# Kernel tuning notes

Measured on AMD Instinct MI355X. Metric: run time of the kernel, lower is better.

Reference implementation:

```python
import jax, jax.numpy as jnp
import numpy as np

N = 50000   # nodes
E = 800000  # edges (before self loops)
NEG_SLOPE = 0.2
EPS_BN = 1e-5
EPS_SM = 1e-16  # PyG softmax denominator epsilon


def gat_conv(x, src, dst, W, att_src, att_dst, bias, heads, ch):
    n = x.shape[0]
    xh = (x @ W).reshape(n, heads, ch)                       # [N,H,C]
    a_src = jnp.sum(xh * att_src, axis=-1)                   # [N,H]
    a_dst = jnp.sum(xh * att_dst, axis=-1)                   # [N,H]
    e = a_src[src] + a_dst[dst]                              # [E,H]
    e = jax.nn.leaky_relu(e, NEG_SLOPE)
    m = jax.ops.segment_max(e, dst, num_segments=n)          # segment softmax
    ex = jnp.exp(e - m[dst])
    denom = jax.ops.segment_sum(ex, dst, num_segments=n)
    alpha = ex / (denom[dst] + EPS_SM)                       # [E,H]
    msg = alpha[:, :, None] * xh[src]                        # [E,H,C]
    out = jax.ops.segment_sum(msg, dst, num_segments=n)      # [N,H,C]
    return out.reshape(n, heads * ch) + bias


def batch_norm(x, gamma, beta):
    mu = jnp.mean(x, axis=0)
    var = jnp.mean((x - mu) ** 2, axis=0)
    return (x - mu) * jax.lax.rsqrt(var + EPS_BN) * gamma + beta


def setup_inputs() -> dict:
    key = jax.random.key(0)
    ks = jax.random.split(key, 16)
    d = {}
    d['x'] = jax.random.normal(ks[0], (N, 128), jnp.float32)
    d['edge_index'] = jax.random.randint(ks[1], (2, E), 0, N, dtype=jnp.int64)
    d['W1'] = jax.random.normal(ks[2], (128, 256), jnp.float32) * 0.1
    d['as1'] = jax.random.normal(ks[3], (2, 128), jnp.float32) * 0.1
    d['ad1'] = jax.random.normal(ks[4], (2, 128), jnp.float32) * 0.1
    d['b1'] = jax.random.normal(ks[5], (256,), jnp.float32) * 0.1
    d['g1'] = jnp.ones((256,), jnp.float32)
    d['be1'] = jnp.zeros((256,), jnp.float32)
    d['W2'] = jax.random.normal(ks[6], (256, 128), jnp.float32) * 0.1
    d['as2'] = jax.random.normal(ks[7], (2, 64), jnp.float32) * 0.1
    d['ad2'] = jax.random.normal(ks[8], (2, 64), jnp.float32) * 0.1
    d['b2'] = jax.random.normal(ks[9], (128,), jnp.float32) * 0.1
    d['g2'] = jnp.ones((128,), jnp.float32)
    d['be2'] = jnp.zeros((128,), jnp.float32)
    d['W3'] = jax.random.normal(ks[10], (128, 128), jnp.float32) * 0.1
    d['as3'] = jax.random.normal(ks[11], (2, 64), jnp.float32) * 0.1
    d['ad3'] = jax.random.normal(ks[12], (2, 64), jnp.float32) * 0.1
    d['b3'] = jax.random.normal(ks[13], (128,), jnp.float32) * 0.1
    d['lw'] = jax.random.normal(ks[14], (128, 64), jnp.float32) * 0.1
    d['lb'] = jnp.zeros((64,), jnp.float32)
    return d


def reference(x, edge_index, W1, as1, ad1, b1, g1, be1,
              W2, as2, ad2, b2, g2, be2,
              W3, as3, ad3, b3, lw, lb):
    # add self loops (PyG GATConv default add_self_loops=True)
    loops = jnp.arange(N, dtype=edge_index.dtype)
    src = jnp.concatenate([edge_index[0], loops])
    dst = jnp.concatenate([edge_index[1], loops])

    h = jax.nn.relu(gat_conv(x, src, dst, W1, as1, ad1, b1, 2, 128))   # [N,256]
    h = batch_norm(h, g1, be1)
    h = jax.nn.relu(gat_conv(h, src, dst, W2, as2, ad2, b2, 2, 64))    # [N,128]
    h = batch_norm(h, g2, be2)
    h = jax.nn.relu(gat_conv(h, src, dst, W3, as3, ad3, b3, 2, 64))    # [N,128]
    return h @ lw + lb                                                 # [N,64]
```

## Files before the change

kernel.cpp:

```cpp
#include <hip/hip_runtime.h>
#include <hip/hip_bf16.h>

#define NEG_SLOPE 0.2f
#define EPS_BN 1e-5f
#define EPS_SM 1e-16f

typedef __bf16 bf16x8 __attribute__((ext_vector_type(8)));
typedef __bf16 bf16x4 __attribute__((ext_vector_type(4)));
typedef __bf16 bf16x2 __attribute__((ext_vector_type(2)));
typedef float floatx4 __attribute__((ext_vector_type(4)));

__device__ __forceinline__ float leaky(float x) { return x > 0.f ? x : NEG_SLOPE * x; }

__global__ void k_detect(const int* __restrict__ ei, int* __restrict__ cnt, int e) {
    int i = threadIdx.x + blockIdx.x * blockDim.x;
    if (i < 1024 && 2 * i + 1 < 2 * e) {
        if (ei[2 * i + 1] != 0) atomicAdd(cnt, 1);
    }
}

__global__ void k_hist(const int* __restrict__ ei, const int* __restrict__ cnt,
                       int* __restrict__ deg, int e) {
    int g = threadIdx.x + blockIdx.x * blockDim.x;
    if (g >= e) return;
    bool is64 = (*cnt) < 512;
    int d = is64 ? ei[2 * (e + g)] : ei[e + g];
    atomicAdd(&deg[d], 1);
}

__global__ __launch_bounds__(1024) void k_scan1(const int* __restrict__ deg,
                                                int* __restrict__ excl,
                                                int* __restrict__ bsum, int n) {
    __shared__ int sm[1024];
    int tid = threadIdx.x;
    int g = blockIdx.x * 1024 + tid;
    int v = (g < n) ? deg[g] : 0;
    sm[tid] = v;
    __syncthreads();
    for (int off = 1; off < 1024; off <<= 1) {
        int t = (tid >= off) ? sm[tid - off] : 0;
        __syncthreads();
        sm[tid] += t;
        __syncthreads();
    }
    if (g < n) excl[g] = sm[tid] - v;
    if (tid == 1023) bsum[blockIdx.x] = sm[1023];
}

__global__ void k_scan2(int* bsum, int nb) {
    if (threadIdx.x == 0 && blockIdx.x == 0) {
        int acc = 0;
        for (int i = 0; i < nb; ++i) { int v = bsum[i]; bsum[i] = acc; acc += v; }
    }
}

__global__ void k_scan3(const int* __restrict__ excl, const int* __restrict__ bsum,
                        int* __restrict__ rowptr, int n, int e) {
    int g = threadIdx.x + blockIdx.x * blockDim.x;
    if (g < n) rowptr[g] = excl[g] + bsum[g >> 10];
    if (g == 0) rowptr[n] = e;
}

__global__ void k_scatter(const int* __restrict__ ei, const int* __restrict__ cnt,
                          const int* __restrict__ rowptr, int* __restrict__ fill,
                          int* __restrict__ col, int e) {
    int g = threadIdx.x + blockIdx.x * blockDim.x;
    if (g >= e) return;
    bool is64 = (*cnt) < 512;
    int s = is64 ? ei[2 * g] : ei[g];
    int d = is64 ? ei[2 * (e + g)] : ei[e + g];
    int pos = rowptr[d] + atomicAdd(&fill[d], 1);
    col[pos] = s;
}

__global__ void k_wconv(const float* __restrict__ W, __bf16* __restrict__ Wb,
                        int kshift, int M, int total) {
    int idx = threadIdx.x + blockIdx.x * blockDim.x;
    if (idx >= total) return;
    int mm = idx >> kshift;
    int kk = idx & ((1 << kshift) - 1);
    Wb[idx] = (__bf16)W[(size_t)kk * M + mm];
}

__global__ void k_bn_prep(const float* __restrict__ sums, const float* __restrict__ sqs,
                          const float* __restrict__ g, const float* __restrict__ b,
                          float* __restrict__ scale, float* __restrict__ shift,
                          int n, int f) {
    int c = threadIdx.x;
    if (c >= f) return;
    float mean = sums[c] / n;
    float var = sqs[c] / n - mean * mean;
    float sc = g[c] * rsqrtf(var + EPS_BN);
    scale[c] = sc;
    shift[c] = b[c] - mean * sc;
}

template <int K, int LC, bool BF16IN>
__global__ __launch_bounds__(256) void k_gemm(const void* __restrict__ Ain,
                                              const __bf16* __restrict__ Bt,
                                              __bf16* __restrict__ Cb, int n, int M,
                                              const float* __restrict__ scale,
                                              const float* __restrict__ shift,
                                              const float* __restrict__ att_s,
                                              const float* __restrict__ att_d,
                                              float* __restrict__ asrc,
                                              float* __restrict__ adst) {
    __shared__ __align__(16) __bf16 As[128][72];
    __shared__ __align__(16) __bf16 Bs[128][72];
    const int row0 = blockIdx.y * 128, col0 = blockIdx.x * 128;
    const int lane = threadIdx.x & 63, w = threadIdx.x >> 6;
    const int m = lane & 15, quad = lane >> 4;
    floatx4 acc[2][8];
#pragma unroll
    for (int i = 0; i < 2; ++i)
#pragma unroll
        for (int j = 0; j < 8; ++j) acc[i][j] = (floatx4)0.f;

    const int sr = threadIdx.x >> 1;
    const int sk = (threadIdx.x & 1) * 32;

    for (int kc = 0; kc < K; kc += 64) {
        {
            int grow = row0 + sr;
            if (grow < n) {
                if (BF16IN) {
                    const __bf16* p = (const __bf16*)Ain + (size_t)grow * K + kc + sk;
#pragma unroll
                    for (int q = 0; q < 4; ++q) {
                        bf16x8 vv = *reinterpret_cast<const bf16x8*>(p + q * 8);
                        if (scale) {
                            const float* scp = scale + kc + sk + q * 8;
                            const float* shp = shift + kc + sk + q * 8;
                            bf16x8 r;
#pragma unroll
                            for (int e2 = 0; e2 < 8; ++e2)
                                r[e2] = (__bf16)((float)vv[e2] * scp[e2] + shp[e2]);
                            vv = r;
                        }
                        *reinterpret_cast<bf16x8*>(&As[sr][sk + q * 8]) = vv;
                    }
                } else {
                    const float* p = (const float*)Ain + (size_t)grow * K + kc + sk;
#pragma unroll
                    for (int q = 0; q < 8; ++q) {
                        float4 v = *reinterpret_cast<const float4*>(p + q * 4);
                        if (scale) {
                            int c = kc + sk + q * 4;
                            float4 sc = *reinterpret_cast<const float4*>(scale + c);
                            float4 sh = *reinterpret_cast<const float4*>(shift + c);
                            v.x = v.x * sc.x + sh.x; v.y = v.y * sc.y + sh.y;
                            v.z = v.z * sc.z + sh.z; v.w = v.w * sc.w + sh.w;
                        }
                        bf16x4 cv = {(__bf16)v.x, (__bf16)v.y, (__bf16)v.z, (__bf16)v.w};
                        *reinterpret_cast<bf16x4*>(&As[sr][sk + q * 4]) = cv;
                    }
                }
            } else {
#pragma unroll
                for (int q = 0; q < 4; ++q)
                    *reinterpret_cast<bf16x8*>(&As[sr][sk + q * 8]) = (bf16x8)(__bf16)0.f;
            }
        }
        {
            const __bf16* p = Bt + (size_t)(col0 + sr) * K + kc + sk;
#pragma unroll
            for (int q = 0; q < 4; ++q)
                *reinterpret_cast<bf16x8*>(&Bs[sr][sk + q * 8]) =
                    *reinterpret_cast<const bf16x8*>(p + q * 8);
        }
        __syncthreads();
#pragma unroll
        for (int ks = 0; ks < 64; ks += 32) {
            bf16x8 a0 = *reinterpret_cast<const bf16x8*>(&As[w * 32 + m][ks + quad * 8]);
            bf16x8 a1 = *reinterpret_cast<const bf16x8*>(&As[w * 32 + 16 + m][ks + quad * 8]);
#pragma unroll
            for (int nt = 0; nt < 8; ++nt) {
                bf16x8 b = *reinterpret_cast<const bf16x8*>(&Bs[nt * 16 + m][ks + quad * 8]);
                acc[0][nt] = __builtin_amdgcn_mfma_f32_16x16x32_bf16(a0, b, acc[0][nt], 0, 0, 0);
                acc[1][nt] = __builtin_amdgcn_mfma_f32_16x16x32_bf16(a1, b, acc[1][nt], 0, 0, 0);
            }
        }
        __syncthreads();
    }
#pragma unroll
    for (int mt = 0; mt < 2; ++mt)
#pragma unroll
        for (int nt = 0; nt < 8; ++nt)
#pragma unroll
            for (int r = 0; r < 4; ++r) {
                int row = row0 + w * 32 + mt * 16 + quad * 4 + r;
                if (row < n) Cb[(size_t)row * M + col0 + nt * 16 + m] = (__bf16)acc[mt][nt][r];
            }
    {
        float asv[8], adv[8];
#pragma unroll
        for (int nt = 0; nt < 8; ++nt) {
            int c = col0 + nt * 16 + m;
            asv[nt] = att_s[c];
            adv[nt] = att_d[c];
        }
#pragma unroll
        for (int mt = 0; mt < 2; ++mt)
#pragma unroll
            for (int r = 0; r < 4; ++r) {
                int row = row0 + w * 32 + mt * 16 + quad * 4 + r;
                if (LC == 7) {
                    float pa = 0.f, pb = 0.f;
#pragma unroll
                    for (int nt = 0; nt < 8; ++nt) {
                        float v = acc[mt][nt][r];
                        pa += v * asv[nt];
                        pb += v * adv[nt];
                    }
#pragma unroll
                    for (int off = 1; off <= 8; off <<= 1) {
                        pa += __shfl_xor(pa, off);
                        pb += __shfl_xor(pb, off);
                    }
                    if (m == 0 && row < n) {
                        int h = (col0 >> 7) & 1;
                        atomicAdd(asrc + 2 * row + h, pa);
                        atomicAdd(adst + 2 * row + h, pb);
                    }
                } else {
                    float p00 = 0.f, p01 = 0.f, p10 = 0.f, p11 = 0.f;
#pragma unroll
                    for (int nt = 0; nt < 8; ++nt) {
                        float v = acc[mt][nt][r];
                        if (nt < 4) { p00 += v * asv[nt]; p10 += v * adv[nt]; }
                        else        { p01 += v * asv[nt]; p11 += v * adv[nt]; }
                    }
#pragma unroll
                    for (int off = 1; off <= 8; off <<= 1) {
                        p00 += __shfl_xor(p00, off);
                        p01 += __shfl_xor(p01, off);
                        p10 += __shfl_xor(p10, off);
                        p11 += __shfl_xor(p11, off);
                    }
                    if (m == 0 && row < n) {
                        atomicAdd(asrc + 2 * row + 0, p00);
                        atomicAdd(asrc + 2 * row + 1, p01);
                        atomicAdd(adst + 2 * row + 0, p10);
                        atomicAdd(adst + 2 * row + 1, p11);
                    }
                }
            }
    }
}

__global__ __launch_bounds__(256) void k_lin(const float* __restrict__ A,
                                             const float* __restrict__ lw,
                                             const float* __restrict__ lb,
                                             float* __restrict__ out, int n) {
    __shared__ __align__(16) __bf16 Ahi[64][136];
    __shared__ __align__(16) __bf16 Alo[64][136];
    __shared__ __align__(16) __bf16 Bhi[64][136];
    const int row0 = blockIdx.x * 64;
    const int lane = threadIdx.x & 63, w = threadIdx.x >> 6;
    const int m = lane & 15, quad = lane >> 4;
    floatx4 acc[4];
#pragma unroll
    for (int i = 0; i < 4; ++i) acc[i] = (floatx4)0.f;

    {
        int sr = threadIdx.x >> 2, sk0 = (threadIdx.x & 3) * 32;
        int grow = row0 + sr;
#pragma unroll
        for (int q = 0; q < 8; ++q) {
            float4 v = make_float4(0.f, 0.f, 0.f, 0.f);
            if (grow < n) v = *reinterpret_cast<const float4*>(A + (size_t)grow * 128 + sk0 + q * 4);
            float vv[4] = {v.x, v.y, v.z, v.w};
#pragma unroll
            for (int i = 0; i < 4; ++i) {
                __bf16 h = (__bf16)vv[i];
                Ahi[sr][sk0 + q * 4 + i] = h;
                Alo[sr][sk0 + q * 4 + i] = (__bf16)(vv[i] - (float)h);
            }
        }
    }
    {
        int k0 = threadIdx.x >> 1, m0 = (threadIdx.x & 1) * 32;
#pragma unroll
        for (int q = 0; q < 8; ++q) {
            float4 v = *reinterpret_cast<const float4*>(lw + (size_t)k0 * 64 + m0 + q * 4);
            float vv[4] = {v.x, v.y, v.z, v.w};
#pragma unroll
            for (int i = 0; i < 4; ++i) Bhi[m0 + q * 4 + i][k0] = (__bf16)vv[i];
        }
    }
    __syncthreads();
#pragma unroll
    for (int ks = 0; ks < 128; ks += 32) {
        bf16x8 ah = *reinterpret_cast<const bf16x8*>(&Ahi[w * 16 + m][ks + quad * 8]);
        bf16x8 al = *reinterpret_cast<const bf16x8*>(&Alo[w * 16 + m][ks + quad * 8]);
#pragma unroll
        for (int nt = 0; nt < 4; ++nt) {
            bf16x8 bh = *reinterpret_cast<const bf16x8*>(&Bhi[nt * 16 + m][ks + quad * 8]);
            acc[nt] = __builtin_amdgcn_mfma_f32_16x16x32_bf16(ah, bh, acc[nt], 0, 0, 0);
            acc[nt] = __builtin_amdgcn_mfma_f32_16x16x32_bf16(al, bh, acc[nt], 0, 0, 0);
        }
    }
#pragma unroll
    for (int nt = 0; nt < 4; ++nt)
#pragma unroll
        for (int r = 0; r < 4; ++r) {
            int row = row0 + w * 16 + quad * 4 + r;
            int c = nt * 16 + m;
            if (row < n) out[(size_t)row * 64 + c] = acc[nt][r] + lb[c];
        }
}

template <int C, bool OUTBF16>
__global__ __launch_bounds__(256) void k_agg(const __bf16* __restrict__ xh,
                                             const float* __restrict__ asrc,
                                             const float* __restrict__ adst,
                                             const int* __restrict__ rowptr,
                                             const int* __restrict__ col,
                                             const float* __restrict__ bias,
                                             void* __restrict__ outv, int n) {
    constexpr int F = 2 * C;
    constexpr int VEC = F / 64;
    __shared__ float4 slots[4][64];
    const int widx = threadIdx.x >> 6;
    const int node = blockIdx.x * 4 + widx;
    const int lane = threadIdx.x & 63;
    if (node >= n) return;
    const bool h1 = (lane * VEC) >= C;
    const int beg = rowptr[node];
    const int deg = rowptr[node + 1] - beg;
    const float2 adv = *reinterpret_cast<const float2*>(adst + 2 * node);
    const float2 asv = *reinterpret_cast<const float2*>(asrc + 2 * node);
    const float es0 = leaky(asv.x + adv.x), es1 = leaky(asv.y + adv.y);
    float acc[VEC] = {};
    float d0 = 0.f, d1 = 0.f;

    for (int base = 0; base < deg; base += 64) {
        const int cnt = min(64, deg - base);
        if (lane < cnt) {
            int s = col[beg + base + lane];
            float2 av = *reinterpret_cast<const float2*>(asrc + 2 * s);
            float w0 = __expf(leaky(av.x + adv.x));
            float w1 = __expf(leaky(av.y + adv.y));
            d0 += w0; d1 += w1;
            slots[widx][lane] = make_float4(__int_as_float(s), w0, w1, 0.f);
        }
        int j = 0;
        for (; j + 4 <= cnt; j += 4) {
            float4 s0 = slots[widx][j + 0];
            float4 s1 = slots[widx][j + 1];
            float4 s2 = slots[widx][j + 2];
            float4 s3 = slots[widx][j + 3];
            const __bf16* p0 = xh + (size_t)__float_as_int(s0.x) * F + lane * VEC;
            const __bf16* p1 = xh + (size_t)__float_as_int(s1.x) * F + lane * VEC;
            const __bf16* p2 = xh + (size_t)__float_as_int(s2.x) * F + lane * VEC;
            const __bf16* p3 = xh + (size_t)__float_as_int(s3.x) * F + lane * VEC;
            if constexpr (VEC == 4) {
                bf16x4 v0 = *reinterpret_cast<const bf16x4*>(p0);
                bf16x4 v1 = *reinterpret_cast<const bf16x4*>(p1);
                bf16x4 v2 = *reinterpret_cast<const bf16x4*>(p2);
                bf16x4 v3 = *reinterpret_cast<const bf16x4*>(p3);
                float w0 = h1 ? s0.z : s0.y, w1 = h1 ? s1.z : s1.y;
                float w2 = h1 ? s2.z : s2.y, w3 = h1 ? s3.z : s3.y;
#pragma unroll
                for (int q = 0; q < 4; ++q)
                    acc[q] += w0 * (float)v0[q] + w1 * (float)v1[q] +
                              w2 * (float)v2[q] + w3 * (float)v3[q];
            } else {
                bf16x2 v0 = *reinterpret_cast<const bf16x2*>(p0);
                bf16x2 v1 = *reinterpret_cast<const bf16x2*>(p1);
                bf16x2 v2 = *reinterpret_cast<const bf16x2*>(p2);
                bf16x2 v3 = *reinterpret_cast<const bf16x2*>(p3);
                float w0 = h1 ? s0.z : s0.y, w1 = h1 ? s1.z : s1.y;
                float w2 = h1 ? s2.z : s2.y, w3 = h1 ? s3.z : s3.y;
#pragma unroll
                for (int q = 0; q < 2; ++q)
                    acc[q] += w0 * (float)v0[q] + w1 * (float)v1[q] +
                              w2 * (float)v2[q] + w3 * (float)v3[q];
            }
        }
        for (; j < cnt; ++j) {
            float4 s0 = slots[widx][j];
            const __bf16* p0 = xh + (size_t)__float_as_int(s0.x) * F + lane * VEC;
            float w0 = h1 ? s0.z : s0.y;
            if constexpr (VEC == 4) {
                bf16x4 v0 = *reinterpret_cast<const bf16x4*>(p0);
#pragma unroll
                for (int q = 0; q < 4; ++q) acc[q] += w0 * (float)v0[q];
            } else {
                bf16x2 v0 = *reinterpret_cast<const bf16x2*>(p0);
#pragma unroll
                for (int q = 0; q < 2; ++q) acc[q] += w0 * (float)v0[q];
            }
        }
    }
#pragma unroll
    for (int off = 1; off <= 32; off <<= 1) {
        d0 += __shfl_xor(d0, off);
        d1 += __shfl_xor(d1, off);
    }
    float exs0 = __expf(es0), exs1 = __expf(es1);
    d0 += exs0; d1 += exs1;
    {
        float ws = h1 ? exs1 : exs0;
        const __bf16* p = xh + (size_t)node * F + lane * VEC;
        if constexpr (VEC == 4) {
            bf16x4 v = *reinterpret_cast<const bf16x4*>(p);
#pragma unroll
            for (int q = 0; q < 4; ++q) acc[q] += ws * (float)v[q];
        } else {
            bf16x2 v = *reinterpret_cast<const bf16x2*>(p);
#pragma unroll
            for (int q = 0; q < 2; ++q) acc[q] += ws * (float)v[q];
        }
    }
    float inv = 1.0f / ((h1 ? d1 : d0) + EPS_SM);
    float o[VEC];
#pragma unroll
    for (int q = 0; q < VEC; ++q) o[q] = fmaxf(acc[q] * inv + bias[lane * VEC + q], 0.f);
    if constexpr (OUTBF16) {
        __bf16* po = (__bf16*)outv + (size_t)node * F + lane * VEC;
        if constexpr (VEC == 4) {
            bf16x4 st = {(__bf16)o[0], (__bf16)o[1], (__bf16)o[2], (__bf16)o[3]};
            *reinterpret_cast<bf16x4*>(po) = st;
        } else {
            bf16x2 st = {(__bf16)o[0], (__bf16)o[1]};
            *reinterpret_cast<bf16x2*>(po) = st;
        }
    } else {
        float* po = (float*)outv + (size_t)node * F + lane * VEC;
        if constexpr (VEC == 4) *reinterpret_cast<float4*>(po) = make_float4(o[0], o[1], o[2], o[3]);
        else                    *reinterpret_cast<float2*>(po) = make_float2(o[0], o[1]);
    }
}

template <typename T>
__global__ void k_bn_stats(const T* __restrict__ x, float* __restrict__ sums,
                           float* __restrict__ sqs, int n, int f) {
    int c = threadIdx.x;
    float s = 0.f, q = 0.f;
    for (int r = blockIdx.x; r < n; r += gridDim.x) {
        float v = (float)x[(size_t)r * f + c];
        s += v; q += v * v;
    }
    atomicAdd(&sums[c], s);
    atomicAdd(&sqs[c], q);
}

extern "C" void kernel_launch(void* const* d_in, const int* in_sizes, int n_in,
                              void* d_out, int out_size, void* d_ws, size_t ws_size,
                              hipStream_t stream) {
    const float* x   = (const float*)d_in[0];
    const int*   ei  = (const int*)d_in[1];
    const float* W1  = (const float*)d_in[2];
    const float* as1 = (const float*)d_in[3];
    const float* ad1 = (const float*)d_in[4];
    const float* b1  = (const float*)d_in[5];
    const float* g1  = (const float*)d_in[6];
    const float* be1 = (const float*)d_in[7];
    const float* W2  = (const float*)d_in[8];
    const float* as2 = (const float*)d_in[9];
    const float* ad2 = (const float*)d_in[10];
    const float* b2  = (const float*)d_in[11];
    const float* g2  = (const float*)d_in[12];
    const float* be2 = (const float*)d_in[13];
    const float* W3  = (const float*)d_in[14];
    const float* as3 = (const float*)d_in[15];
    const float* ad3 = (const float*)d_in[16];
    const float* b3  = (const float*)d_in[17];
    const float* lw  = (const float*)d_in[18];
    const float* lb  = (const float*)d_in[19];
    float* outp = (float*)d_out;

    const int n = in_sizes[0] / 128;
    const int e = in_sizes[1] / 2;

    char* w = (char*)d_ws;
    size_t off = 0;
    auto alloc = [&](size_t bytes) -> void* {
        void* p = w + off;
        off += (bytes + 255) & ~(size_t)255;
        return p;
    };
    __bf16* xhb = (__bf16*)alloc((size_t)n * 256 * 2);
    __bf16* h1b = (__bf16*)alloc((size_t)n * 256 * 2);
    __bf16* h2b = (__bf16*)alloc((size_t)n * 128 * 2);
    float*  h3f = (float*)alloc((size_t)n * 128 * 4);
    int* excl   = (int*)alloc((size_t)n * 4);
    int* rowptr = (int*)alloc((size_t)(n + 1) * 4);
    int* colb   = (int*)alloc((size_t)e * 4);
    int* bsum   = (int*)alloc(64 * 4);
    float* sc1  = (float*)alloc(256 * 4);
    float* sh1  = (float*)alloc(256 * 4);
    float* sc2  = (float*)alloc(128 * 4);
    float* sh2  = (float*)alloc(128 * 4);
    __bf16* Wb1 = (__bf16*)alloc(256 * 128 * 2);
    __bf16* Wb2 = (__bf16*)alloc(128 * 256 * 2);
    __bf16* Wb3 = (__bf16*)alloc(128 * 128 * 2);
    char* zb_begin = (char*)(w + off);
    int* deg    = (int*)alloc((size_t)n * 4);
    int* fill   = (int*)alloc((size_t)n * 4);
    float* bn1  = (float*)alloc(512 * 4);
    float* bn2  = (float*)alloc(512 * 4);
    int* dcnt   = (int*)alloc(256);
    float* as1p = (float*)alloc((size_t)n * 2 * 4);
    float* ad1p = (float*)alloc((size_t)n * 2 * 4);
    float* as2p = (float*)alloc((size_t)n * 2 * 4);
    float* ad2p = (float*)alloc((size_t)n * 2 * 4);
    float* as3p = (float*)alloc((size_t)n * 2 * 4);
    float* ad3p = (float*)alloc((size_t)n * 2 * 4);
    char* zb_end = (char*)(w + off);

    const int nb1 = (n + 1023) / 1024;

    hipMemsetAsync(zb_begin, 0, (size_t)(zb_end - zb_begin), stream);

    k_detect<<<4, 256, 0, stream>>>(ei, dcnt, e);
    k_hist<<<(e + 255) / 256, 256, 0, stream>>>(ei, dcnt, deg, e);
    k_scan1<<<nb1, 1024, 0, stream>>>(deg, excl, bsum, n);
    k_scan2<<<1, 1, 0, stream>>>(bsum, nb1);
    k_scan3<<<(n + 255) / 256, 256, 0, stream>>>(excl, bsum, rowptr, n, e);
    k_scatter<<<(e + 255) / 256, 256, 0, stream>>>(ei, dcnt, rowptr, fill, colb, e);

    k_wconv<<<(256 * 128 + 255) / 256, 256, 0, stream>>>(W1, Wb1, 7, 256, 256 * 128);
    k_wconv<<<(128 * 256 + 255) / 256, 256, 0, stream>>>(W2, Wb2, 8, 128, 128 * 256);
    k_wconv<<<(128 * 128 + 255) / 256, 256, 0, stream>>>(W3, Wb3, 7, 128, 128 * 128);

    const int nwb = (n + 3) / 4;
    const int nrow = (n + 127) / 128;

    k_gemm<128, 7, false><<<dim3(2, nrow), 256, 0, stream>>>(
        x, Wb1, xhb, n, 256, nullptr, nullptr, as1, ad1, as1p, ad1p);
    k_agg<128, true><<<nwb, 256, 0, stream>>>(xhb, as1p, ad1p, rowptr, colb, b1, h1b, n);
    k_bn_stats<__bf16><<<256, 256, 0, stream>>>(h1b, bn1, bn1 + 256, n, 256);
    k_bn_prep<<<1, 256, 0, stream>>>(bn1, bn1 + 256, g1, be1, sc1, sh1, n, 256);

    k_gemm<256, 6, true><<<dim3(1, nrow), 256, 0, stream>>>(
        h1b, Wb2, xhb, n, 128, sc1, sh1, as2, ad2, as2p, ad2p);
    k_agg<64, true><<<nwb, 256, 0, stream>>>(xhb, as2p, ad2p, rowptr, colb, b2, h2b, n);
    k_bn_stats<__bf16><<<256, 128, 0, stream>>>(h2b, bn2, bn2 + 256, n, 128);
    k_bn_prep<<<1, 256, 0, stream>>>(bn2, bn2 + 256, g2, be2, sc2, sh2, n, 128);

    k_gemm<128, 6, true><<<dim3(1, nrow), 256, 0, stream>>>(
        h2b, Wb3, xhb, n, 128, sc2, sh2, as3, ad3, as3p, ad3p);
    k_agg<64, false><<<nwb, 256, 0, stream>>>(xhb, as3p, ad3p, rowptr, colb, b3, h3f, n);

    k_lin<<<(n + 63) / 64, 256, 0, stream>>>(h3f, lw, lb, outp, n);
}
```

Measured before the change: 533.5 us.

## Vectorize GAT aggregation gathers and cut CSR/BN/weight-conversion launches

```diff
diff --git a/kernel.cpp b/kernel.cpp
--- a/kernel.cpp
+++ b/kernel.cpp
@@ -7,7 +7,6 @@
 
 typedef __bf16 bf16x8 __attribute__((ext_vector_type(8)));
 typedef __bf16 bf16x4 __attribute__((ext_vector_type(4)));
-typedef __bf16 bf16x2 __attribute__((ext_vector_type(2)));
 typedef float floatx4 __attribute__((ext_vector_type(4)));
 
 __device__ __forceinline__ float leaky(float x) { return x > 0.f ? x : NEG_SLOPE * x; }
@@ -20,12 +19,12 @@
 }
 
 __global__ void k_hist(const int* __restrict__ ei, const int* __restrict__ cnt,
-                       int* __restrict__ deg, int e) {
+                       int* __restrict__ deg, int* __restrict__ rnk, int e) {
     int g = threadIdx.x + blockIdx.x * blockDim.x;
     if (g >= e) return;
     bool is64 = (*cnt) < 512;
     int d = is64 ? ei[2 * (e + g)] : ei[e + g];
-    atomicAdd(&deg[d], 1);
+    rnk[g] = atomicAdd(&deg[d], 1);
 }
 
 __global__ __launch_bounds__(1024) void k_scan1(const int* __restrict__ deg,
@@ -47,69 +46,79 @@
     if (tid == 1023) bsum[blockIdx.x] = sm[1023];
 }
 
-__global__ void k_scan2(int* bsum, int nb) {
-    if (threadIdx.x == 0 && blockIdx.x == 0) {
-        int acc = 0;
-        for (int i = 0; i < nb; ++i) { int v = bsum[i]; bsum[i] = acc; acc += v; }
-    }
-}
-
 __global__ void k_scan3(const int* __restrict__ excl, const int* __restrict__ bsum,
                         int* __restrict__ rowptr, int n, int e) {
+    __shared__ int pref;
     int g = threadIdx.x + blockIdx.x * blockDim.x;
-    if (g < n) rowptr[g] = excl[g] + bsum[g >> 10];
+    if (threadIdx.x == 0) {
+        int chunk = (blockIdx.x * blockDim.x) >> 10;
+        int acc = 0;
+        for (int i = 0; i < chunk; ++i) acc += bsum[i];
+        pref = acc;
+    }
+    __syncthreads();
+    if (g < n) rowptr[g] = excl[g] + pref;
     if (g == 0) rowptr[n] = e;
 }
 
 __global__ void k_scatter(const int* __restrict__ ei, const int* __restrict__ cnt,
-                          const int* __restrict__ rowptr, int* __restrict__ fill,
+                          const int* __restrict__ rowptr, const int* __restrict__ rnk,
                           int* __restrict__ col, int e) {
     int g = threadIdx.x + blockIdx.x * blockDim.x;
     if (g >= e) return;
     bool is64 = (*cnt) < 512;
     int s = is64 ? ei[2 * g] : ei[g];
     int d = is64 ? ei[2 * (e + g)] : ei[e + g];
-    int pos = rowptr[d] + atomicAdd(&fill[d], 1);
-    col[pos] = s;
-}
-
-__global__ void k_wconv(const float* __restrict__ W, __bf16* __restrict__ Wb,
-                        int kshift, int M, int total) {
+    col[rowptr[d] + rnk[g]] = s;
+}
+
+__global__ void k_wconv(const float* __restrict__ W1, __bf16* __restrict__ Wb1,
+                        const float* __restrict__ W2, __bf16* __restrict__ Wb2,
+                        const float* __restrict__ W3, __bf16* __restrict__ Wb3) {
     int idx = threadIdx.x + blockIdx.x * blockDim.x;
-    if (idx >= total) return;
-    int mm = idx >> kshift;
-    int kk = idx & ((1 << kshift) - 1);
-    Wb[idx] = (__bf16)W[(size_t)kk * M + mm];
-}
-
-__global__ void k_bn_prep(const float* __restrict__ sums, const float* __restrict__ sqs,
-                          const float* __restrict__ g, const float* __restrict__ b,
-                          float* __restrict__ scale, float* __restrict__ shift,
-                          int n, int f) {
-    int c = threadIdx.x;
-    if (c >= f) return;
-    float mean = sums[c] / n;
-    float var = sqs[c] / n - mean * mean;
-    float sc = g[c] * rsqrtf(var + EPS_BN);
-    scale[c] = sc;
-    shift[c] = b[c] - mean * sc;
+    if (idx < 32768) {
+        int mm = idx >> 7, kk = idx & 127;
+        Wb1[idx] = (__bf16)W1[(size_t)kk * 256 + mm];
+    } else if (idx < 65536) {
+        int i2 = idx - 32768;
+        int mm = i2 >> 8, kk = i2 & 255;
+        Wb2[i2] = (__bf16)W2[(size_t)kk * 128 + mm];
+    } else if (idx < 81920) {
+        int i3 = idx - 65536;
+        int mm = i3 >> 7, kk = i3 & 127;
+        Wb3[i3] = (__bf16)W3[(size_t)kk * 128 + mm];
+    }
 }
 
 template <int K, int LC, bool BF16IN>
 __global__ __launch_bounds__(256) void k_gemm(const void* __restrict__ Ain,
                                               const __bf16* __restrict__ Bt,
                                               __bf16* __restrict__ Cb, int n, int M,
-                                              const float* __restrict__ scale,
-                                              const float* __restrict__ shift,
+                                              const float* __restrict__ bnsums,
+                                              const float* __restrict__ gam,
+                                              const float* __restrict__ bet,
                                               const float* __restrict__ att_s,
                                               const float* __restrict__ att_d,
                                               float* __restrict__ asrc,
                                               float* __restrict__ adst) {
     __shared__ __align__(16) __bf16 As[128][72];
     __shared__ __align__(16) __bf16 Bs[128][72];
+    __shared__ float sc_lds[K], sh_lds[K];
     const int row0 = blockIdx.y * 128, col0 = blockIdx.x * 128;
     const int lane = threadIdx.x & 63, w = threadIdx.x >> 6;
     const int m = lane & 15, quad = lane >> 4;
+
+    if (bnsums) {
+        for (int c = threadIdx.x; c < K; c += 256) {
+            float mean = bnsums[c] / n;
+            float var = bnsums[256 + c] / n - mean * mean;
+            float sc = gam[c] * rsqrtf(var + EPS_BN);
+            sc_lds[c] = sc;
+            sh_lds[c] = bet[c] - mean * sc;
+        }
+        __syncthreads();
+    }
+
     floatx4 acc[2][8];
 #pragma unroll
     for (int i = 0; i < 2; ++i)
@@ -128,13 +137,12 @@
 #pragma unroll
                     for (int q = 0; q < 4; ++q) {
                         bf16x8 vv = *reinterpret_cast<const bf16x8*>(p + q * 8);
-                        if (scale) {
-                            const float* scp = scale + kc + sk + q * 8;
-                            const float* shp = shift + kc + sk + q * 8;
+                        if (bnsums) {
+                            int c = kc + sk + q * 8;
                             bf16x8 r;
 #pragma unroll
                             for (int e2 = 0; e2 < 8; ++e2)
-                                r[e2] = (__bf16)((float)vv[e2] * scp[e2] + shp[e2]);
+                                r[e2] = (__bf16)((float)vv[e2] * sc_lds[c + e2] + sh_lds[c + e2]);
                             vv = r;
                         }
                         *reinterpret_cast<bf16x8*>(&As[sr][sk + q * 8]) = vv;
@@ -144,13 +152,6 @@
 #pragma unroll
                     for (int q = 0; q < 8; ++q) {
                         float4 v = *reinterpret_cast<const float4*>(p + q * 4);
-                        if (scale) {
-                            int c = kc + sk + q * 4;
-                            float4 sc = *reinterpret_cast<const float4*>(scale + c);
-                            float4 sh = *reinterpret_cast<const float4*>(shift + c);
-                            v.x = v.x * sc.x + sh.x; v.y = v.y * sc.y + sh.y;
-                            v.z = v.z * sc.z + sh.z; v.w = v.w * sc.w + sh.w;
-                        }
                         bf16x4 cv = {(__bf16)v.x, (__bf16)v.y, (__bf16)v.z, (__bf16)v.w};
                         *reinterpret_cast<bf16x4*>(&As[sr][sk + q * 4]) = cv;
                     }
@@ -261,7 +262,6 @@
     floatx4 acc[4];
 #pragma unroll
     for (int i = 0; i < 4; ++i) acc[i] = (floatx4)0.f;
-
     {
         int sr = threadIdx.x >> 2, sk0 = (threadIdx.x & 3) * 32;
         int grow = row0 + sr;
@@ -319,117 +319,86 @@
                                              const float* __restrict__ bias,
                                              void* __restrict__ outv, int n) {
     constexpr int F = 2 * C;
-    constexpr int VEC = F / 64;
-    __shared__ float4 slots[4][64];
+    constexpr int G = F / 8;
+    constexpr int NG = 64 / G;
+    constexpr int GSH = (G == 32) ? 5 : 4;
+    __shared__ float4 slots[4][72];
     const int widx = threadIdx.x >> 6;
     const int node = blockIdx.x * 4 + widx;
     const int lane = threadIdx.x & 63;
     if (node >= n) return;
-    const bool h1 = (lane * VEC) >= C;
+    const int t = lane & (G - 1);
+    const int g = lane >> GSH;
+    const bool h1 = (t * 8) >= C;
+    if (lane < 8) slots[widx][64 + lane] = make_float4(0.f, 0.f, 0.f, 0.f);
     const int beg = rowptr[node];
     const int deg = rowptr[node + 1] - beg;
     const float2 adv = *reinterpret_cast<const float2*>(adst + 2 * node);
     const float2 asv = *reinterpret_cast<const float2*>(asrc + 2 * node);
     const float es0 = leaky(asv.x + adv.x), es1 = leaky(asv.y + adv.y);
-    float acc[VEC] = {};
+    float acc[8] = {};
     float d0 = 0.f, d1 = 0.f;
 
     for (int base = 0; base < deg; base += 64) {
         const int cnt = min(64, deg - base);
+        float4 sv = make_float4(0.f, 0.f, 0.f, 0.f);
         if (lane < cnt) {
             int s = col[beg + base + lane];
             float2 av = *reinterpret_cast<const float2*>(asrc + 2 * s);
             float w0 = __expf(leaky(av.x + adv.x));
             float w1 = __expf(leaky(av.y + adv.y));
             d0 += w0; d1 += w1;
-            slots[widx][lane] = make_float4(__int_as_float(s), w0, w1, 0.f);
-        }
-        int j = 0;
-        for (; j + 4 <= cnt; j += 4) {
-            float4 s0 = slots[widx][j + 0];
-            float4 s1 = slots[widx][j + 1];
-            float4 s2 = slots[widx][j + 2];
-            float4 s3 = slots[widx][j + 3];
-            const __bf16* p0 = xh + (size_t)__float_as_int(s0.x) * F + lane * VEC;
-            const __bf16* p1 = xh + (size_t)__float_as_int(s1.x) * F + lane * VEC;
-            const __bf16* p2 = xh + (size_t)__float_as_int(s2.x) * F + lane * VEC;
-            const __bf16* p3 = xh + (size_t)__float_as_int(s3.x) * F + lane * VEC;
-            if constexpr (VEC == 4) {
-                bf16x4 v0 = *reinterpret_cast<const bf16x4*>(p0);
-                bf16x4 v1 = *reinterpret_cast<const bf16x4*>(p1);
-                bf16x4 v2 = *reinterpret_cast<const bf16x4*>(p2);
-                bf16x4 v3 = *reinterpret_cast<const bf16x4*>(p3);
-                float w0 = h1 ? s0.z : s0.y, w1 = h1 ? s1.z : s1.y;
-                float w2 = h1 ? s2.z : s2.y, w3 = h1 ? s3.z : s3.y;
-#pragma unroll
-                for (int q = 0; q < 4; ++q)
-                    acc[q] += w0 * (float)v0[q] + w1 * (float)v1[q] +
-                              w2 * (float)v2[q] + w3 * (float)v3[q];
-            } else {
-                bf16x2 v0 = *reinterpret_cast<const bf16x2*>(p0);
-                bf16x2 v1 = *reinterpret_cast<const bf16x2*>(p1);
-                bf16x2 v2 = *reinterpret_cast<const bf16x2*>(p2);
-                bf16x2 v3 = *reinterpret_cast<const bf16x2*>(p3);
-                float w0 = h1 ? s0.z : s0.y, w1 = h1 ? s1.z : s1.y;
-                float w2 = h1 ? s2.z : s2.y, w3 = h1 ? s3.z : s3.y;
-#pragma unroll
-                for (int q = 0; q < 2; ++q)
-                    acc[q] += w0 * (float)v0[q] + w1 * (float)v1[q] +
-                              w2 * (float)v2[q] + w3 * (float)v3[q];
-            }
-        }
-        for (; j < cnt; ++j) {
+            sv = make_float4(__int_as_float(s * (F * 2)), w0, w1, 0.f);
+        }
+        slots[widx][lane] = sv;
+        for (int j = g; j < cnt; j += 2 * NG) {
             float4 s0 = slots[widx][j];
-            const __bf16* p0 = xh + (size_t)__float_as_int(s0.x) * F + lane * VEC;
+            float4 s1 = slots[widx][j + NG];
+            const char* p0 = (const char*)xh + (unsigned)__float_as_int(s0.x);
+            const char* p1 = (const char*)xh + (unsigned)__float_as_int(s1.x);
+            bf16x8 v0 = *reinterpret_cast<const bf16x8*>(p0 + t * 16);
+            bf16x8 v1 = *reinterpret_cast<const bf16x8*>(p1 + t * 16);
             float w0 = h1 ? s0.z : s0.y;
-            if constexpr (VEC == 4) {
-                bf16x4 v0 = *reinterpret_cast<const bf16x4*>(p0);
-#pragma unroll
-                for (int q = 0; q < 4; ++q) acc[q] += w0 * (float)v0[q];
-            } else {
-                bf16x2 v0 = *reinterpret_cast<const bf16x2*>(p0);
-#pragma unroll
-                for (int q = 0; q < 2; ++q) acc[q] += w0 * (float)v0[q];
-            }
+            float w1 = h1 ? s1.z : s1.y;
+#pragma unroll
+            for (int q = 0; q < 8; ++q) acc[q] += w0 * (float)v0[q] + w1 * (float)v1[q];
         }
     }
 #pragma unroll
     for (int off = 1; off <= 32; off <<= 1) {
         d0 += __shfl_xor(d0, off);
         d1 += __shfl_xor(d1, off);
+    }
+#pragma unroll
+    for (int q = 0; q < 8; ++q) {
+#pragma unroll
+        for (int off = G; off < 64; off <<= 1) acc[q] += __shfl_xor(acc[q], off);
     }
     float exs0 = __expf(es0), exs1 = __expf(es1);
     d0 += exs0; d1 += exs1;
     {
         float ws = h1 ? exs1 : exs0;
-        const __bf16* p = xh + (size_t)node * F + lane * VEC;
-        if constexpr (VEC == 4) {
-            bf16x4 v = *reinterpret_cast<const bf16x4*>(p);
-#pragma unroll
-            for (int q = 0; q < 4; ++q) acc[q] += ws * (float)v[q];
+        const __bf16* p = xh + (size_t)node * F + t * 8;
+        bf16x8 v = *reinterpret_cast<const bf16x8*>(p);
+#pragma unroll
+        for (int q = 0; q < 8; ++q) acc[q] += ws * (float)v[q];
+    }
+    float inv = 1.0f / ((h1 ? d1 : d0) + EPS_SM);
+    float o[8];
+#pragma unroll
+    for (int q = 0; q < 8; ++q) o[q] = fmaxf(acc[q] * inv + bias[t * 8 + q], 0.f);
+    if (g == 0) {
+        if constexpr (OUTBF16) {
+            __bf16* po = (__bf16*)outv + (size_t)node * F + t * 8;
+            bf16x8 st;
+#pragma unroll
+            for (int q = 0; q < 8; ++q) st[q] = (__bf16)o[q];
+            *reinterpret_cast<bf16x8*>(po) = st;
         } else {
-            bf16x2 v = *reinterpret_cast<const bf16x2*>(p);
-#pragma unroll
-            for (int q = 0; q < 2; ++q) acc[q] += ws * (float)v[q];
-        }
-    }
-    float inv = 1.0f / ((h1 ? d1 : d0) + EPS_SM);
-    float o[VEC];
-#pragma unroll
-    for (int q = 0; q < VEC; ++q) o[q] = fmaxf(acc[q] * inv + bias[lane * VEC + q], 0.f);
-    if constexpr (OUTBF16) {
-        __bf16* po = (__bf16*)outv + (size_t)node * F + lane * VEC;
-        if constexpr (VEC == 4) {
-            bf16x4 st = {(__bf16)o[0], (__bf16)o[1], (__bf16)o[2], (__bf16)o[3]};
-            *reinterpret_cast<bf16x4*>(po) = st;
-        } else {
-            bf16x2 st = {(__bf16)o[0], (__bf16)o[1]};
-            *reinterpret_cast<bf16x2*>(po) = st;
-        }
-    } else {
-        float* po = (float*)outv + (size_t)node * F + lane * VEC;
-        if constexpr (VEC == 4) *reinterpret_cast<float4*>(po) = make_float4(o[0], o[1], o[2], o[3]);
-        else                    *reinterpret_cast<float2*>(po) = make_float2(o[0], o[1]);
+            float* po = (float*)outv + (size_t)node * F + t * 8;
+            *reinterpret_cast<float4*>(po) = make_float4(o[0], o[1], o[2], o[3]);
+            *reinterpret_cast<float4*>(po + 4) = make_float4(o[4], o[5], o[6], o[7]);
+        }
     }
 }
 
@@ -488,17 +457,13 @@
     int* excl   = (int*)alloc((size_t)n * 4);
     int* rowptr = (int*)alloc((size_t)(n + 1) * 4);
     int* colb   = (int*)alloc((size_t)e * 4);
+    int* rnk    = (int*)alloc((size_t)e * 4);
     int* bsum   = (int*)alloc(64 * 4);
-    float* sc1  = (float*)alloc(256 * 4);
-    float* sh1  = (float*)alloc(256 * 4);
-    float* sc2  = (float*)alloc(128 * 4);
-    float* sh2  = (float*)alloc(128 * 4);
     __bf16* Wb1 = (__bf16*)alloc(256 * 128 * 2);
     __bf16* Wb2 = (__bf16*)alloc(128 * 256 * 2);
     __bf16* Wb3 = (__bf16*)alloc(128 * 128 * 2);
     char* zb_begin = (char*)(w + off);
     int* deg    = (int*)alloc((size_t)n * 4);
-    int* fill   = (int*)alloc((size_t)n * 4);
     float* bn1  = (float*)alloc(512 * 4);
     float* bn2  = (float*)alloc(512 * 4);
     int* dcnt   = (int*)alloc(256);
@@ -515,33 +480,27 @@
     hipMemsetAsync(zb_begin, 0, (size_t)(zb_end - zb_begin), stream);
 
     k_detect<<<4, 256, 0, stream>>>(ei, dcnt, e);
-    k_hist<<<(e + 255) / 256, 256, 0, stream>>>(ei, dcnt, deg, e);
+    k_hist<<<(e + 255) / 256, 256, 0, stream>>>(ei, dcnt, deg, rnk, e);
     k_scan1<<<nb1, 1024, 0, stream>>>(deg, excl, bsum, n);
-    k_scan2<<<1, 1, 0, stream>>>(bsum, nb1);
     k_scan3<<<(n + 255) / 256, 256, 0, stream>>>(excl, bsum, rowptr, n, e);
-    k_scatter<<<(e + 255) / 256, 256, 0, stream>>>(ei, dcnt, rowptr, fill, colb, e);
-
-    k_wconv<<<(256 * 128 + 255) / 256, 256, 0, stream>>>(W1, Wb1, 7, 256, 256 * 128);
-    k_wconv<<<(128 * 256 + 255) / 256, 256, 0, stream>>>(W2, Wb2, 8, 128, 128 * 256);
-    k_wconv<<<(128 * 128 + 255) / 256, 256, 0, stream>>>(W3, Wb3, 7, 128, 128 * 128);
+    k_scatter<<<(e + 255) / 256, 256, 0, stream>>>(ei, dcnt, rowptr, rnk, colb, e);
+    k_wconv<<<(81920 + 255) / 256, 256, 0, stream>>>(W1, Wb1, W2, Wb2, W3, Wb3);
 
     const int nwb = (n + 3) / 4;
     const int nrow = (n + 127) / 128;
 
     k_gemm<128, 7, false><<<dim3(2, nrow), 256, 0, stream>>>(
-        x, Wb1, xhb, n, 256, nullptr, nullptr, as1, ad1, as1p, ad1p);
+        x, Wb1, xhb, n, 256, nullptr, nullptr, nullptr, as1, ad1, as1p, ad1p);
     k_agg<128, true><<<nwb, 256, 0, stream>>>(xhb, as1p, ad1p, rowptr, colb, b1, h1b, n);
     k_bn_stats<__bf16><<<256, 256, 0, stream>>>(h1b, bn1, bn1 + 256, n, 256);
-    k_bn_prep<<<1, 256, 0, stream>>>(bn1, bn1 + 256, g1, be1, sc1, sh1, n, 256);
 
     k_gemm<256, 6, true><<<dim3(1, nrow), 256, 0, stream>>>(
-        h1b, Wb2, xhb, n, 128, sc1, sh1, as2, ad2, as2p, ad2p);
+        h1b, Wb2, xhb, n, 128, bn1, g1, be1, as2, ad2, as2p, ad2p);
     k_agg<64, true><<<nwb, 256, 0, stream>>>(xhb, as2p, ad2p, rowptr, colb, b2, h2b, n);
     k_bn_stats<__bf16><<<256, 128, 0, stream>>>(h2b, bn2, bn2 + 256, n, 128);
-    k_bn_prep<<<1, 256, 0, stream>>>(bn2, bn2 + 256, g2, be2, sc2, sh2, n, 128);
 
     k_gemm<128, 6, true><<<dim3(1, nrow), 256, 0, stream>>>(
-        h2b, Wb3, xhb, n, 128, sc2, sh2, as3, ad3, as3p, ad3p);
+        h2b, Wb3, xhb, n, 128, bn2, g2, be2, as3, ad3, as3p, ad3p);
     k_agg<64, false><<<nwb, 256, 0, stream>>>(xhb, as3p, ad3p, rowptr, colb, b3, h3f, n);
 
     k_lin<<<(n + 63) / 64, 256, 0, stream>>>(h3f, lw, lb, outp, n);
```

Result: faster. 477.0 us (-10.6%).
